# Kernel optimization log

Measured on AMD Instinct MI355X. Metric: run time of the kernel, lower is better.

## Reference

```python
import jax, jax.numpy as jnp
import numpy as np

B, C, H, W = 32, 256, 64, 64
LN_EPS = 1e-5

def _conv1x1(x, w, b=None):
    # x: (b,c,h,w), w: (out,c) -> (b,out,h,w)
    y = jnp.einsum('bchw,oc->bohw', x, w)
    if b is not None:
        y = y + b[None, :, None, None]
    return y

def _hsigmoid(t):
    # mmcv HSigmoid: clamp((x + 3) / 6, 0, 1)
    return jnp.clip((t + 3.0) / 6.0, 0.0, 1.0)

def setup_inputs() -> dict:
    key = jax.random.key(0)
    ks = jax.random.split(key, 12)
    s = 0.05
    return {
        'x': jax.random.normal(ks[0], (B, C, H, W), jnp.float32),
        'conv0_w': jax.random.normal(ks[1], (C // 2, C), jnp.float32) * s,
        'conv0_b': jnp.zeros((C // 2,), jnp.float32),
        'bn1_w': jax.random.normal(ks[2], (C, C // 2), jnp.float32) * s,
        'bn1_b': jnp.zeros((C,), jnp.float32),
        'conv1_w': jax.random.normal(ks[3], (1, C), jnp.float32) * s,
        'conv1_b': jnp.zeros((1,), jnp.float32),
        'ln_g': jnp.ones((C,), jnp.float32),
        'ln_b': jnp.zeros((C,), jnp.float32),
        'sk_w1': jax.random.normal(ks[4], (C // 2, C), jnp.float32) * s,
        'sk_w2': jax.random.normal(ks[5], (C, C // 2), jnp.float32) * s,
        'res_w': jax.random.normal(ks[6], (C, C), jnp.float32) * s,
        'res_b': jnp.zeros((C,), jnp.float32),
    }

def reference(x, conv0_w, conv0_b, bn1_w, bn1_b, conv1_w, conv1_b,
              ln_g, ln_b, sk_w1, sk_w2, res_w, res_b):
    b, c, h, w = x.shape
    # ---- channel attention ----
    ca = _conv1x1(x, conv0_w, conv0_b)               # (b, c/2, h, w)
    ca = ca.mean(axis=(2, 3), keepdims=True)          # GAP -> (b, c/2, 1, 1)
    ca = _conv1x1(ca, bn1_w, bn1_b)                   # (b, c, 1, 1)
    ca = _hsigmoid(ca)
    v = ca.reshape(b, c)                              # nchw_to_nlc -> (b, 1, c); LN over c
    mu = v.mean(axis=-1, keepdims=True)
    var = ((v - mu) ** 2).mean(axis=-1, keepdims=True)
    v = (v - mu) * jax.lax.rsqrt(var + LN_EPS) * ln_g + ln_b
    ca = v.reshape(b, c, 1, 1)
    # ---- spatial attention ----
    sa = _conv1x1(x, conv1_w, conv1_b)                # (b, 1, h, w)
    # ---- parallel attention ----
    par = _hsigmoid(sa + ca)                          # (b, c, h, w)
    # ---- sequence attention: bmm outer product (b,c,1)x(b,1,hw) ----
    seq = _hsigmoid(ca * sa)                          # (b, c, h, w)
    # ---- SK module ----
    u = (seq + par).mean(axis=(2, 3), keepdims=True)  # GAP -> (b, c, 1, 1)
    u = _conv1x1(u, sk_w1)                            # (b, c/2, 1, 1), no bias
    u = _conv1x1(u, sk_w2)                            # (b, c, 1, 1), no bias
    a = jax.nn.softmax(u, axis=1)
    sk = seq * a + par * (1.0 - a)
    # softmax over spatial (nchw_to_nlc + Softmax(dim=1))
    sk = jax.nn.softmax(sk.reshape(b, c, h * w), axis=2).reshape(b, c, h, w)
    selected = x * sk
    # ---- self attention ----
    self_attn = selected.sum(axis=(2, 3)).reshape(b, c, 1, 1) + _conv1x1(x, res_w, res_b)
    return selected + self_attn
```

## Files before the change

kernel.cpp:

```cpp
#include <hip/hip_runtime.h>
#include <math.h>

#define B_  32
#define C_  256
#define HW_ 4096
#define LN_EPS 1e-5f

typedef __attribute__((ext_vector_type(4))) float f32x4;
typedef __attribute__((ext_vector_type(8))) short bf16x8;
typedef __attribute__((ext_vector_type(4))) unsigned u32x4;
typedef __attribute__((ext_vector_type(2))) unsigned u32x2;

__device__ __forceinline__ float hsig(float v) {
    return fminf(fmaxf((v + 3.0f) * (1.0f / 6.0f), 0.0f), 1.0f);
}
__device__ __forceinline__ float tval(float ca, float a, float sav) {
    return a * hsig(ca * sav) + (1.0f - a) * hsig(ca + sav);
}
__device__ __forceinline__ unsigned short f2bf(float f) {
    unsigned u = __float_as_uint(f);
    unsigned r = (u + 0x7fffu + ((u >> 16) & 1u)) >> 16;
    return (unsigned short)r;
}
__device__ __forceinline__ float bf2f(unsigned short h) {
    return __uint_as_float(((unsigned)h) << 16);
}
__device__ __forceinline__ int bswz(int n) {
    return ((n & 7) ^ ((n >> 3) & 7)) << 4;
}


__global__ __launch_bounds__(1024) void k_pass1c(
    const float* __restrict__ x, const float* __restrict__ w1,
    float* __restrict__ sa, float* __restrict__ xs_part,
    unsigned short* __restrict__ xbf)
{
    __shared__ float sw1[C_];
    __shared__ float sred[16][256];
    __shared__ float xsl[C_];
    int hwq = blockIdx.x, b = blockIdx.y;
    int tid = threadIdx.x, w = tid >> 6, l = tid & 63;
    int hw0 = hwq * 256;
    if (tid < 256) sw1[tid] = w1[tid];
    __syncthreads();
    const float* xb = x + (size_t)b * (C_ * HW_) + hw0 + l * 4;
    unsigned short* xo = xbf + (size_t)b * (C_ * HW_) + hw0 + l * 4;
    f32x4 sacc = {0.f, 0.f, 0.f, 0.f};
    #pragma unroll 4
    for (int i = 0; i < 16; ++i) {
        int c = i * 16 + w;
        f32x4 v = *(const f32x4*)(xb + (size_t)c * HW_);
        sacc += sw1[c] * v;
        ushort4 o = { f2bf(v.x), f2bf(v.y), f2bf(v.z), f2bf(v.w) };
        *(ushort4*)(xo + (size_t)c * HW_) = o;
        float h = (v.x + v.y) + (v.z + v.w);
        h += __shfl_xor(h, 32); h += __shfl_xor(h, 16); h += __shfl_xor(h, 8);
        h += __shfl_xor(h, 4);  h += __shfl_xor(h, 2);  h += __shfl_xor(h, 1);
        if (l == 0) xsl[c] = h;
    }
    *(f32x4*)&sred[w][l * 4] = sacc;
    __syncthreads();
    if (tid < 256) {
        float s = 0.f;
        #pragma unroll
        for (int g = 0; g < 16; ++g) s += sred[g][tid];
        sa[(size_t)b * HW_ + hw0 + tid] = s;
        xs_part[((size_t)hwq * B_ + b) * C_ + tid] = xsl[tid];
    }
}

__global__ void k_ca(const float* __restrict__ xs_part, const float* __restrict__ w0,
                     const float* __restrict__ b0, const float* __restrict__ w1,
                     const float* __restrict__ b1, const float* __restrict__ g,
                     const float* __restrict__ be, float* __restrict__ ca,
                     const float* __restrict__ rw, unsigned short* __restrict__ wbs,
                     int nparts) {
    int b = blockIdx.x, tid = threadIdx.x;
    __shared__ float xm[C_], t0[128], red[4];
    float xs = 0.f;
    for (int i = 0; i < nparts; ++i)
        xs += xs_part[((size_t)i * B_ + b) * C_ + tid];
    xm[tid] = xs * (1.0f / HW_);
    __syncthreads();
    if (tid < 128) {
        float s = b0[tid];
        const float* wr = w0 + tid * C_;
        for (int c = 0; c < C_; ++c) s += wr[c] * xm[c];
        t0[tid] = s;
    }
    __syncthreads();
    float s = b1[tid];
    const float* wr = w1 + tid * 128;
    for (int o = 0; o < 128; ++o) s += wr[o] * t0[o];
    float v = hsig(s);
    float sum = v;
    #pragma unroll
    for (int o = 32; o; o >>= 1) sum += __shfl_xor(sum, o);
    if ((tid & 63) == 0) red[tid >> 6] = sum;
    __syncthreads();
    float mu = (red[0] + red[1] + red[2] + red[3]) * (1.0f / C_);
    __syncthreads();
    float d = v - mu;
    float sq = d * d;
    #pragma unroll
    for (int o = 32; o; o >>= 1) sq += __shfl_xor(sq, o);
    if ((tid & 63) == 0) red[tid >> 6] = sq;
    __syncthreads();
    float var = (red[0] + red[1] + red[2] + red[3]) * (1.0f / C_);
    ca[b * C_ + tid] = d * (1.0f / sqrtf(var + LN_EPS)) * g[tid] + be[tid];

    int gid = b * 256 + tid;
    int lane = gid & 63;
    int mi = (gid >> 6) & 3;
    int ks = (gid >> 8) & 7;
    int wv2 = gid >> 11;
    int m = wv2 * 64 + mi * 16 + (lane & 15);
    int kb = ks * 32 + (lane >> 4) * 8;
    const float* src = rw + m * C_ + kb;
    f32x4 a4 = *(const f32x4*)src;
    f32x4 b4 = *(const f32x4*)(src + 4);
    ushort4 o0 = { f2bf(a4.x), f2bf(a4.y), f2bf(a4.z), f2bf(a4.w) };
    ushort4 o1 = { f2bf(b4.x), f2bf(b4.y), f2bf(b4.z), f2bf(b4.w) };
    unsigned short* dst = wbs + (size_t)gid * 8;
    *(ushort4*)dst = o0;
    *(ushort4*)(dst + 4) = o1;
}

__global__ void k_u2(const float* __restrict__ sa, const float* __restrict__ ca,
                     const float* __restrict__ b1, float* __restrict__ u) {
    int bc = blockIdx.x;
    int b = bc >> 7, c0 = (bc & 127) * 2;
    int tid = threadIdx.x;
    float ca0 = ca[b * C_ + c0], ca1 = ca[b * C_ + c0 + 1];
    float bias = b1[0];
    const float* sp = sa + (size_t)b * HW_;
    float s0 = 0.f, s1 = 0.f;
    for (int i = 0; i < 16; ++i) {
        f32x4 v = *(const f32x4*)(sp + i * 256 + tid * 4);
        #pragma unroll
        for (int j = 0; j < 4; ++j) {
            float sv = v[j] + bias;
            s0 += hsig(ca0 * sv) + hsig(ca0 + sv);
            s1 += hsig(ca1 * sv) + hsig(ca1 + sv);
        }
    }
    #pragma unroll
    for (int o = 32; o; o >>= 1) { s0 += __shfl_xor(s0, o); s1 += __shfl_xor(s1, o); }
    if (tid == 0) {
        u[b * C_ + c0]     = s0 * (1.0f / HW_);
        u[b * C_ + c0 + 1] = s1 * (1.0f / HW_);
    }
}

__global__ void k_a(const float* __restrict__ u, const float* __restrict__ w1,
                    const float* __restrict__ w2, float* __restrict__ aout) {
    int b = blockIdx.x, tid = threadIdx.x;
    __shared__ float uu[C_], v0[128], red[4];
    uu[tid] = u[b * C_ + tid];
    __syncthreads();
    if (tid < 128) {
        float s = 0.f;
        const float* wr = w1 + tid * C_;
        for (int c = 0; c < C_; ++c) s += wr[c] * uu[c];
        v0[tid] = s;
    }
    __syncthreads();
    float s = 0.f;
    const float* wr = w2 + tid * 128;
    for (int o = 0; o < 128; ++o) s += wr[o] * v0[o];
    float m = s;
    #pragma unroll
    for (int o = 32; o; o >>= 1) m = fmaxf(m, __shfl_xor(m, o));
    if ((tid & 63) == 0) red[tid >> 6] = m;
    __syncthreads();
    m = fmaxf(fmaxf(red[0], red[1]), fmaxf(red[2], red[3]));
    __syncthreads();
    float e = __expf(s - m);
    float se = e;
    #pragma unroll
    for (int o = 32; o; o >>= 1) se += __shfl_xor(se, o);
    if ((tid & 63) == 0) red[tid >> 6] = se;
    __syncthreads();
    float tot = red[0] + red[1] + red[2] + red[3];
    aout[b * C_ + tid] = e / tot;
}

__global__ void k_stats4(const unsigned short* __restrict__ xbf, const float* __restrict__ sa,
                         const float* __restrict__ b1,
                         const float* __restrict__ ca, const float* __restrict__ aw,
                         const float* __restrict__ res_b, f32x4* __restrict__ st4) {
    int blk = blockIdx.x;
    int b = blk >> 7, c0 = (blk & 127) * 2;
    int bc0 = b * C_ + c0;
    int tid = threadIdx.x;
    float ca0 = ca[bc0],     a0 = aw[bc0];
    float ca1 = ca[bc0 + 1], a1 = aw[bc0 + 1];
    float bias = b1[0];
    const float* sp = sa + (size_t)b * HW_;
    const unsigned* xp0 = (const unsigned*)(xbf + (size_t)bc0 * HW_);
    const unsigned* xp1 = (const unsigned*)(xbf + (size_t)(bc0 + 1) * HW_);
    float se0 = 0.f, xe0 = 0.f, se1 = 0.f, xe1 = 0.f;
    #pragma unroll
    for (int i = 0; i < 4; ++i) {
        f32x4 s4 = *(const f32x4*)(sp + i * 1024 + tid * 4);
        u32x2 xa = *(const u32x2*)(xp0 + i * 512 + tid * 2);
        u32x2 xc = *(const u32x2*)(xp1 + i * 512 + tid * 2);
        float va[4], vc[4];
        va[0] = bf2f((unsigned short)(xa[0] & 0xffffu));
        va[1] = bf2f((unsigned short)(xa[0] >> 16));
        va[2] = bf2f((unsigned short)(xa[1] & 0xffffu));
        va[3] = bf2f((unsigned short)(xa[1] >> 16));
        vc[0] = bf2f((unsigned short)(xc[0] & 0xffffu));
        vc[1] = bf2f((unsigned short)(xc[0] >> 16));
        vc[2] = bf2f((unsigned short)(xc[1] & 0xffffu));
        vc[3] = bf2f((unsigned short)(xc[1] >> 16));
        #pragma unroll
        for (int j = 0; j < 4; ++j) {
            float sv = s4[j] + bias;
            float e0 = __expf(tval(ca0, a0, sv));
            float e1 = __expf(tval(ca1, a1, sv));
            se0 += e0; xe0 += va[j] * e0;
            se1 += e1; xe1 += vc[j] * e1;
        }
    }
    __shared__ float red[4][4];
    #pragma unroll
    for (int o = 32; o; o >>= 1) {
        se0 += __shfl_xor(se0, o); xe0 += __shfl_xor(xe0, o);
        se1 += __shfl_xor(se1, o); xe1 += __shfl_xor(xe1, o);
    }
    if ((tid & 63) == 0) {
        int w = tid >> 6;
        red[0][w] = se0; red[1][w] = xe0; red[2][w] = se1; red[3][w] = xe1;
    }
    __syncthreads();
    if (tid == 0) {
        float S0 = red[0][0] + red[0][1] + red[0][2] + red[0][3];
        float X0 = red[1][0] + red[1][1] + red[1][2] + red[1][3];
        float S1 = red[2][0] + red[2][1] + red[2][2] + red[2][3];
        float X1 = red[3][0] + red[3][1] + red[3][2] + red[3][3];
        float r0 = 1.0f / S0, r1 = 1.0f / S1;
        f32x4 st0 = { ca0, a0, r0, X0 * r0 + res_b[c0] };
        f32x4 st1 = { ca1, a1, r1, X1 * r1 + res_b[c0 + 1] };
        st4[bc0] = st0;
        st4[bc0 + 1] = st1;
    }
}

__global__ __launch_bounds__(256, 3) void k_out3(
    const unsigned short* __restrict__ xbf, const unsigned short* __restrict__ wbs,
    const float* __restrict__ sa, const float* __restrict__ b1,
    const f32x4* __restrict__ st4, float* __restrict__ out)
{
    __shared__ __align__(16) unsigned short Bs[64 * 256];
    __shared__ f32x4 sst[C_];
    __shared__ float ssa[64];

    int b = blockIdx.x, tile = blockIdx.y;
    int n0 = tile * 64;
    int tid = threadIdx.x;
    int w = tid >> 6, lane = tid & 63;
    int hwc = tid & 7;
    int cq  = tid >> 3;

    const unsigned short* xb = xbf + (size_t)b * (C_ * HW_) + n0 + hwc * 8;
    u32x4 ld[2][4];
    #pragma unroll
    for (int it = 0; it < 2; ++it) {
        int c0 = it * 128 + cq * 4;
        #pragma unroll
        for (int r = 0; r < 4; ++r)
            ld[it][r] = *(const u32x4*)(xb + (size_t)(c0 + r) * HW_);
    }

    bf16x8 af[2][4];
    const bf16x8* wp = (const bf16x8*)wbs;
    #pragma unroll
    for (int ks2 = 0; ks2 < 2; ++ks2)
        #pragma unroll
        for (int mi = 0; mi < 4; ++mi)
            af[ks2][mi] = wp[(size_t)(((w * 8 + ks2) * 4 + mi) * 64 + lane)];

    sst[tid] = st4[b * C_ + tid];
    if (tid < 64) ssa[tid] = sa[(size_t)b * HW_ + n0 + tid] + b1[0];

    #pragma unroll
    for (int it = 0; it < 2; ++it) {
        int kp0 = it * 64 + cq * 2;
        #pragma unroll
        for (int e = 0; e < 8; ++e) {
            int n = hwc * 8 + e;
            unsigned a0 = ld[it][0][e >> 1], b0v = ld[it][1][e >> 1];
            unsigned a1 = ld[it][2][e >> 1], b1v = ld[it][3][e >> 1];
            unsigned d0, d1;
            if (e & 1) {
                d0 = (a0 >> 16) | (b0v & 0xffff0000u);
                d1 = (a1 >> 16) | (b1v & 0xffff0000u);
            } else {
                d0 = (a0 & 0xffffu) | (b0v << 16);
                d1 = (a1 & 0xffffu) | (b1v << 16);
            }
            int bo = (n * 512 + kp0 * 4) ^ bswz(n);
            u32x2 dd = { d0, d1 };
            *(u32x2*)((char*)Bs + bo) = dd;
        }
    }
    __syncthreads();

    f32x4 acc[4][4];
    #pragma unroll
    for (int i = 0; i < 4; ++i)
        #pragma unroll
        for (int j = 0; j < 4; ++j) acc[i][j] = (f32x4){0.f, 0.f, 0.f, 0.f};

    #pragma unroll
    for (int ksg = 0; ksg < 4; ++ksg) {
        #pragma unroll
        for (int ks2 = 0; ks2 < 2; ++ks2) {
            int ks = ksg * 2 + ks2;
            bf16x8 bfr[4];
            #pragma unroll
            for (int ni = 0; ni < 4; ++ni) {
                int n = ni * 16 + (lane & 15);
                int bo = (n * 512 + ks * 64 + (lane >> 4) * 16) ^ bswz(n);
                bfr[ni] = *(const bf16x8*)((const char*)Bs + bo);
            }
            #pragma unroll
            for (int mi = 0; mi < 4; ++mi)
                #pragma unroll
                for (int ni = 0; ni < 4; ++ni)
                    acc[mi][ni] = __builtin_amdgcn_mfma_f32_16x16x32_bf16(
                        af[ks2][mi], bfr[ni], acc[mi][ni], 0, 0, 0);
            if (ksg < 3) {
                #pragma unroll
                for (int mi = 0; mi < 4; ++mi)
                    af[ks2][mi] = wp[(size_t)(((w * 8 + (ksg + 1) * 2 + ks2) * 4 + mi) * 64 + lane)];
            }
        }
    }

    float* ob = out + (size_t)b * (C_ * HW_) + n0;
    #pragma unroll
    for (int mi = 0; mi < 4; ++mi) {
        int m0 = w * 64 + mi * 16 + (lane >> 4) * 4;
        f32x4 s0 = sst[m0 + 0];
        f32x4 s1 = sst[m0 + 1];
        f32x4 s2 = sst[m0 + 2];
        f32x4 s3 = sst[m0 + 3];
        #pragma unroll
        for (int ni = 0; ni < 4; ++ni) {
            int n = ni * 16 + (lane & 15);
            float sav = ssa[n];
            int bo = (n * 512 + m0 * 2) ^ bswz(n);
            ushort4 xv = *(const ushort4*)((const char*)Bs + bo);
            float o0 = acc[mi][ni][0] + bf2f(xv.x) * (__expf(tval(s0.x, s0.y, sav)) * s0.z) + s0.w;
            float o1 = acc[mi][ni][1] + bf2f(xv.y) * (__expf(tval(s1.x, s1.y, sav)) * s1.z) + s1.w;
            float o2 = acc[mi][ni][2] + bf2f(xv.z) * (__expf(tval(s2.x, s2.y, sav)) * s2.z) + s2.w;
            float o3 = acc[mi][ni][3] + bf2f(xv.w) * (__expf(tval(s3.x, s3.y, sav)) * s3.z) + s3.w;
            __builtin_nontemporal_store(o0, &ob[(size_t)(m0 + 0) * HW_ + n]);
            __builtin_nontemporal_store(o1, &ob[(size_t)(m0 + 1) * HW_ + n]);
            __builtin_nontemporal_store(o2, &ob[(size_t)(m0 + 2) * HW_ + n]);
            __builtin_nontemporal_store(o3, &ob[(size_t)(m0 + 3) * HW_ + n]);
        }
    }
}


__global__ void k_pass1(const float* __restrict__ x, const float* __restrict__ w1,
                        float* __restrict__ sa, float* __restrict__ xs_part)
{
    int tid = threadIdx.x, wave = tid >> 6, lane = tid & 63;
    int hwq = blockIdx.x, b = blockIdx.y, ct = blockIdx.z;
    int c0 = ct * 32;
    int hw0 = hwq * 1024;
    const float* xb = x + (size_t)b * (C_ * HW_) + hw0 + tid * 4;
    __shared__ float part[32 * 4];
    f32x4 sacc = {0.f, 0.f, 0.f, 0.f};
    #pragma unroll 4
    for (int cc = 0; cc < 32; ++cc) {
        int c = c0 + cc;
        f32x4 v = *(const f32x4*)(xb + (size_t)c * HW_);
        float wv = w1[c];
        sacc += wv * v;
        float h = (v.x + v.y) + (v.z + v.w);
        h += __shfl_xor(h, 32); h += __shfl_xor(h, 16); h += __shfl_xor(h, 8);
        h += __shfl_xor(h, 4);  h += __shfl_xor(h, 2);  h += __shfl_xor(h, 1);
        if (lane == 0) part[cc * 4 + wave] = h;
    }
    float* sp = sa + (size_t)b * HW_ + hw0 + tid * 4;
    atomicAdd(sp + 0, sacc.x);
    atomicAdd(sp + 1, sacc.y);
    atomicAdd(sp + 2, sacc.z);
    atomicAdd(sp + 3, sacc.w);
    __syncthreads();
    if (tid < 32)
        xs_part[((size_t)hwq * B_ + b) * C_ + c0 + tid] =
            part[tid * 4 + 0] + part[tid * 4 + 1] + part[tid * 4 + 2] + part[tid * 4 + 3];
}

__global__ void k_u(const float* __restrict__ sa, const float* __restrict__ ca,
                    const float* __restrict__ b1, float* __restrict__ u) {
    int bc = blockIdx.x;
    int b = bc >> 8;
    int tid = threadIdx.x;
    float cav = ca[bc];
    float bias = b1[0];
    const float* sp = sa + (size_t)b * HW_;
    float s = 0.f;
    for (int i = 0; i < 16; ++i) {
        f32x4 v = *(const f32x4*)(sp + i * 256 + tid * 4);
        #pragma unroll
        for (int j = 0; j < 4; ++j) {
            float sv = v[j] + bias;
            s += hsig(cav * sv) + hsig(cav + sv);
        }
    }
    #pragma unroll
    for (int o = 32; o; o >>= 1) s += __shfl_xor(s, o);
    if (tid == 0) u[bc] = s * (1.0f / HW_);
}

__global__ void k_stats(const float* __restrict__ x, const float* __restrict__ sa,
                        const float* __restrict__ b1,
                        const float* __restrict__ ca, const float* __restrict__ aw,
                        const float* __restrict__ res_b, f32x4* __restrict__ st4) {
    int bc = blockIdx.x;
    int b = bc >> 8, c = bc & 255;
    int tid = threadIdx.x;
    float cav = ca[bc], av = aw[bc];
    float bias = b1[0];
    const float* sp = sa + (size_t)b * HW_;
    const float* xp = x + (size_t)bc * HW_;
    float se = 0.f, xe = 0.f;
    #pragma unroll
    for (int i = 0; i < 4; ++i) {
        f32x4 s4 = *(const f32x4*)(sp + i * 1024 + tid * 4);
        f32x4 x4 = *(const f32x4*)(xp + i * 1024 + tid * 4);
        #pragma unroll
        for (int j = 0; j < 4; ++j) {
            float e = __expf(tval(cav, av, s4[j] + bias));
            se += e;
            xe += x4[j] * e;
        }
    }
    __shared__ float red[4], red2[4];
    #pragma unroll
    for (int o = 32; o; o >>= 1) { se += __shfl_xor(se, o); xe += __shfl_xor(xe, o); }
    if ((tid & 63) == 0) { red[tid >> 6] = se; red2[tid >> 6] = xe; }
    __syncthreads();
    if (tid == 0) {
        float S = red[0] + red[1] + red[2] + red[3];
        float X = red2[0] + red2[1] + red2[2] + red2[3];
        float rcp = 1.0f / S;
        f32x4 st = { cav, av, rcp, X * rcp + res_b[c] };
        st4[bc] = st;
    }
}

__global__ __launch_bounds__(256, 2) void k_out(
    const float* __restrict__ x, const unsigned short* __restrict__ wbs,
    const float* __restrict__ sa, const float* __restrict__ b1,
    const f32x4* __restrict__ st4, float* __restrict__ out)
{
    __shared__ __align__(16) unsigned short Bs[64 * 256];
    __shared__ f32x4 sst[C_];
    __shared__ float ssa[64];

    int b = blockIdx.x, tile = blockIdx.y;
    int n0 = tile * 64;
    int tid = threadIdx.x;
    int w = tid >> 6, lane = tid & 63;

    const float* xb = x + (size_t)b * (C_ * HW_);

    bf16x8 af[8][4];
    #pragma unroll
    for (int ks = 0; ks < 8; ++ks)
        #pragma unroll
        for (int mi = 0; mi < 4; ++mi)
            af[ks][mi] = *(const bf16x8*)(wbs + (size_t)(((w * 8 + ks) * 4 + mi) * 64 + lane) * 8);

    sst[tid] = st4[b * C_ + tid];
    if (tid < 64) ssa[tid] = sa[(size_t)b * HW_ + n0 + tid] + b1[0];

    #pragma unroll
    for (int p2 = 0; p2 < 8; ++p2) {
        int id = p2 * 256 + tid;
        int kp = id >> 4;
        int tcn = id & 15;
        const float* g0 = xb + (size_t)(2 * kp) * HW_ + n0 + 4 * tcn;
        f32x4 v0 = *(const f32x4*)g0;
        f32x4 v1 = *(const f32x4*)(g0 + HW_);
        #pragma unroll
        for (int i = 0; i < 4; ++i) {
            int n = 4 * tcn + i;
            unsigned val = (unsigned)f2bf(v0[i]) | ((unsigned)f2bf(v1[i]) << 16);
            int bo = (n * 512 + kp * 4) ^ ((n & 7) << 4);
            *(unsigned*)((char*)Bs + bo) = val;
        }
    }
    __syncthreads();

    f32x4 acc[4][4];
    #pragma unroll
    for (int i = 0; i < 4; ++i)
        #pragma unroll
        for (int j = 0; j < 4; ++j) acc[i][j] = (f32x4){0.f, 0.f, 0.f, 0.f};

    #pragma unroll
    for (int ks = 0; ks < 8; ++ks) {
        bf16x8 bfr[4];
        #pragma unroll
        for (int ni = 0; ni < 4; ++ni) {
            int n = ni * 16 + (lane & 15);
            int bo = (n * 512 + ks * 64 + (lane >> 4) * 16) ^ ((n & 7) << 4);
            bfr[ni] = *(const bf16x8*)((const char*)Bs + bo);
        }
        #pragma unroll
        for (int mi = 0; mi < 4; ++mi)
            #pragma unroll
            for (int ni = 0; ni < 4; ++ni)
                acc[mi][ni] = __builtin_amdgcn_mfma_f32_16x16x32_bf16(
                    af[ks][mi], bfr[ni], acc[mi][ni], 0, 0, 0);
    }

    float* ob = out + (size_t)b * (C_ * HW_) + n0;
    #pragma unroll
    for (int mi = 0; mi < 4; ++mi) {
        int m0 = w * 64 + mi * 16 + (lane >> 4) * 4;
        f32x4 s0 = sst[m0 + 0];
        f32x4 s1 = sst[m0 + 1];
        f32x4 s2 = sst[m0 + 2];
        f32x4 s3 = sst[m0 + 3];
        #pragma unroll
        for (int ni = 0; ni < 4; ++ni) {
            int n = ni * 16 + (lane & 15);
            float sav = ssa[n];
            int bo = (n * 512 + m0 * 2) ^ ((n & 7) << 4);
            ushort4 xv = *(const ushort4*)((const char*)Bs + bo);
            float o0 = acc[mi][ni][0] + bf2f(xv.x) * (__expf(tval(s0.x, s0.y, sav)) * s0.z) + s0.w;
            float o1 = acc[mi][ni][1] + bf2f(xv.y) * (__expf(tval(s1.x, s1.y, sav)) * s1.z) + s1.w;
            float o2 = acc[mi][ni][2] + bf2f(xv.z) * (__expf(tval(s2.x, s2.y, sav)) * s2.z) + s2.w;
            float o3 = acc[mi][ni][3] + bf2f(xv.w) * (__expf(tval(s3.x, s3.y, sav)) * s3.z) + s3.w;
            ob[(size_t)(m0 + 0) * HW_ + n] = o0;
            ob[(size_t)(m0 + 1) * HW_ + n] = o1;
            ob[(size_t)(m0 + 2) * HW_ + n] = o2;
            ob[(size_t)(m0 + 3) * HW_ + n] = o3;
        }
    }
}

extern "C" void kernel_launch(void* const* d_in, const int* in_sizes, int n_in,
                              void* d_out, int out_size, void* d_ws, size_t ws_size,
                              hipStream_t stream) {
    (void)in_sizes; (void)n_in; (void)out_size;
    const float* x   = (const float*)d_in[0];
    const float* c0w = (const float*)d_in[1];
    const float* c0b = (const float*)d_in[2];
    const float* b1w = (const float*)d_in[3];
    const float* b1b = (const float*)d_in[4];
    const float* c1w = (const float*)d_in[5];
    const float* c1b = (const float*)d_in[6];
    const float* lng = (const float*)d_in[7];
    const float* lnb = (const float*)d_in[8];
    const float* sw1 = (const float*)d_in[9];
    const float* sw2 = (const float*)d_in[10];
    const float* rw  = (const float*)d_in[11];
    const float* rb  = (const float*)d_in[12];
    float* out = (float*)d_out;
    float* ws = (float*)d_ws;

    const size_t NEW_WS_FLOATS = (size_t)352256 + 16777216;
    if (ws_size >= NEW_WS_FLOATS * sizeof(float)) {
        float* sa      = ws;
        float* xs_part = ws + 131072;
        float* ca      = ws + 262144;
        float* u       = ws + 270336;
        float* aw      = ws + 278528;
        f32x4* st4     = (f32x4*)(ws + 286720);
        unsigned short* wbs = (unsigned short*)(ws + 319488);
        unsigned short* xbf = (unsigned short*)(ws + 352256);

        hipLaunchKernelGGL(k_pass1c, dim3(16, 32), dim3(1024), 0, stream, x, c1w, sa, xs_part, xbf);
        hipLaunchKernelGGL(k_ca,     dim3(32),     dim3(256),  0, stream, xs_part, c0w, c0b, b1w, b1b, lng, lnb, ca, rw, wbs, 16);
        hipLaunchKernelGGL(k_u2,     dim3(4096),   dim3(64),   0, stream, sa, ca, c1b, u);
        hipLaunchKernelGGL(k_a,      dim3(32),     dim3(256),  0, stream, u, sw1, sw2, aw);
        hipLaunchKernelGGL(k_stats4, dim3(4096),   dim3(256),  0, stream, xbf, sa, c1b, ca, aw, rb, st4);
        hipLaunchKernelGGL(k_out3,   dim3(32, 64), dim3(256),  0, stream, xbf, wbs, sa, c1b, st4, out);
    } else {
        float* sa      = ws;
        float* xs_part = ws + 131072;
        float* ca      = ws + 163840;
        float* u       = ws + 172032;
        float* aw      = ws + 180224;
        f32x4* st4     = (f32x4*)(ws + 188416);
        unsigned short* wbs = (unsigned short*)(ws + 221184);

        hipMemsetAsync(sa, 0, (size_t)B_ * HW_ * sizeof(float), stream);
        hipLaunchKernelGGL(k_pass1, dim3(4, 32, 8), dim3(256), 0, stream, x, c1w, sa, xs_part);
        hipLaunchKernelGGL(k_ca,    dim3(32),       dim3(256), 0, stream, xs_part, c0w, c0b, b1w, b1b, lng, lnb, ca, rw, wbs, 4);
        hipLaunchKernelGGL(k_u,     dim3(8192),     dim3(64),  0, stream, sa, ca, c1b, u);
        hipLaunchKernelGGL(k_a,     dim3(32),       dim3(256), 0, stream, u, sw1, sw2, aw);
        hipLaunchKernelGGL(k_stats, dim3(8192),     dim3(256), 0, stream, x, sa, c1b, ca, aw, rb, st4);
        hipLaunchKernelGGL(k_out,   dim3(32, 64),   dim3(256), 0, stream, x, wbs, sa, c1b, st4, out);
    }
}
```

Before: 146.1 us.

## Split first pass over channel tiles with atomic accumulation of spatial conv

Replaces the 1024-thread pass-1 kernel, whose blocks each cover all 256 channels for 256 pixels, with 256-thread blocks that each cover 32 channels for 1024 pixels. This gives a grid of 4x32x8. The spatial 1x1 conv partial sums are now combined across channel tiles with float atomics into a zeroed buffer, which needs an extra memset. The intent is more parallel blocks with shorter serial chains and no cross-wave LDS reduction. The cost is atomic traffic and the extra memset launch, and the atomics make the summation order nondeterministic.

After: 158.0 us. 8.1% more time.

```diff
diff --git a/kernel.cpp b/kernel.cpp
--- a/kernel.cpp
+++ b/kernel.cpp
@@ -30,43 +30,40 @@
 }
 
 
-__global__ __launch_bounds__(1024) void k_pass1c(
-    const float* __restrict__ x, const float* __restrict__ w1,
-    float* __restrict__ sa, float* __restrict__ xs_part,
-    unsigned short* __restrict__ xbf)
+__global__ void k_pass1f(const float* __restrict__ x, const float* __restrict__ w1,
+                         float* __restrict__ sa, float* __restrict__ xs_part,
+                         unsigned short* __restrict__ xbf)
 {
-    __shared__ float sw1[C_];
-    __shared__ float sred[16][256];
-    __shared__ float xsl[C_];
-    int hwq = blockIdx.x, b = blockIdx.y;
-    int tid = threadIdx.x, w = tid >> 6, l = tid & 63;
-    int hw0 = hwq * 256;
-    if (tid < 256) sw1[tid] = w1[tid];
-    __syncthreads();
-    const float* xb = x + (size_t)b * (C_ * HW_) + hw0 + l * 4;
-    unsigned short* xo = xbf + (size_t)b * (C_ * HW_) + hw0 + l * 4;
+    int tid = threadIdx.x, wave = tid >> 6, lane = tid & 63;
+    int hwq = blockIdx.x, b = blockIdx.y, ct = blockIdx.z;
+    int c0 = ct * 32;
+    int hw0 = hwq * 1024;
+    const float* xb = x + (size_t)b * (C_ * HW_) + hw0 + tid * 4;
+    unsigned short* xo = xbf + (size_t)b * (C_ * HW_) + hw0 + tid * 4;
+    __shared__ float part[32 * 4];
     f32x4 sacc = {0.f, 0.f, 0.f, 0.f};
     #pragma unroll 4
-    for (int i = 0; i < 16; ++i) {
-        int c = i * 16 + w;
+    for (int cc = 0; cc < 32; ++cc) {
+        int c = c0 + cc;
         f32x4 v = *(const f32x4*)(xb + (size_t)c * HW_);
-        sacc += sw1[c] * v;
+        float wv = w1[c];
+        sacc += wv * v;
         ushort4 o = { f2bf(v.x), f2bf(v.y), f2bf(v.z), f2bf(v.w) };
         *(ushort4*)(xo + (size_t)c * HW_) = o;
         float h = (v.x + v.y) + (v.z + v.w);
         h += __shfl_xor(h, 32); h += __shfl_xor(h, 16); h += __shfl_xor(h, 8);
         h += __shfl_xor(h, 4);  h += __shfl_xor(h, 2);  h += __shfl_xor(h, 1);
-        if (l == 0) xsl[c] = h;
-    }
-    *(f32x4*)&sred[w][l * 4] = sacc;
-    __syncthreads();
-    if (tid < 256) {
-        float s = 0.f;
-        #pragma unroll
-        for (int g = 0; g < 16; ++g) s += sred[g][tid];
-        sa[(size_t)b * HW_ + hw0 + tid] = s;
-        xs_part[((size_t)hwq * B_ + b) * C_ + tid] = xsl[tid];
-    }
+        if (lane == 0) part[cc * 4 + wave] = h;
+    }
+    float* sp = sa + (size_t)b * HW_ + hw0 + tid * 4;
+    atomicAdd(sp + 0, sacc.x);
+    atomicAdd(sp + 1, sacc.y);
+    atomicAdd(sp + 2, sacc.z);
+    atomicAdd(sp + 3, sacc.w);
+    __syncthreads();
+    if (tid < 32)
+        xs_part[((size_t)hwq * B_ + b) * C_ + c0 + tid] =
+            part[tid * 4 + 0] + part[tid * 4 + 1] + part[tid * 4 + 2] + part[tid * 4 + 3];
 }
 
 __global__ void k_ca(const float* __restrict__ xs_part, const float* __restrict__ w0,
@@ -581,12 +578,13 @@
         unsigned short* wbs = (unsigned short*)(ws + 319488);
         unsigned short* xbf = (unsigned short*)(ws + 352256);
 
-        hipLaunchKernelGGL(k_pass1c, dim3(16, 32), dim3(1024), 0, stream, x, c1w, sa, xs_part, xbf);
-        hipLaunchKernelGGL(k_ca,     dim3(32),     dim3(256),  0, stream, xs_part, c0w, c0b, b1w, b1b, lng, lnb, ca, rw, wbs, 16);
-        hipLaunchKernelGGL(k_u2,     dim3(4096),   dim3(64),   0, stream, sa, ca, c1b, u);
-        hipLaunchKernelGGL(k_a,      dim3(32),     dim3(256),  0, stream, u, sw1, sw2, aw);
-        hipLaunchKernelGGL(k_stats4, dim3(4096),   dim3(256),  0, stream, xbf, sa, c1b, ca, aw, rb, st4);
-        hipLaunchKernelGGL(k_out3,   dim3(32, 64), dim3(256),  0, stream, xbf, wbs, sa, c1b, st4, out);
+        hipMemsetAsync(sa, 0, (size_t)B_ * HW_ * sizeof(float), stream);
+        hipLaunchKernelGGL(k_pass1f, dim3(4, 32, 8), dim3(256), 0, stream, x, c1w, sa, xs_part, xbf);
+        hipLaunchKernelGGL(k_ca,     dim3(32),       dim3(256), 0, stream, xs_part, c0w, c0b, b1w, b1b, lng, lnb, ca, rw, wbs, 4);
+        hipLaunchKernelGGL(k_u2,     dim3(4096),     dim3(64),  0, stream, sa, ca, c1b, u);
+        hipLaunchKernelGGL(k_a,      dim3(32),       dim3(256), 0, stream, u, sw1, sw2, aw);
+        hipLaunchKernelGGL(k_stats4, dim3(4096),     dim3(256), 0, stream, xbf, sa, c1b, ca, aw, rb, st4);
+        hipLaunchKernelGGL(k_out3,   dim3(32, 64),   dim3(256), 0, stream, xbf, wbs, sa, c1b, st4, out);
     } else {
         float* sa      = ws;
         float* xs_part = ws + 131072;
```
